# Optimization experiments

Measured on AMD Instinct MI355X. Metric: run time of the kernel, lower is better.

## Reference

```python
import jax, jax.numpy as jnp
import numpy as np

B, L, F = 8, 4096, 64  # batch, max_len, feat_dim (in_features == out_features)


def setup_inputs() -> dict:
    key = jax.random.key(0)
    k1, k2, k3, k4 = jax.random.split(key, 4)
    text = jax.random.normal(k1, (B, L, F), dtype=jnp.float32)
    adj = jax.random.uniform(k2, (B, L, L), dtype=jnp.float32)
    weight = jax.random.normal(k3, (F, F), dtype=jnp.float32) * (1.0 / np.sqrt(F))
    bias = jax.random.normal(k4, (F,), dtype=jnp.float32) * 0.01
    return {"text": text, "adj": adj, "weight": weight, "bias": bias}


def reference(text, adj, weight, bias):
    # Original: out[b,i,:] = sum_j adj[b,i,j] * (text[b,j,:] @ W) + bias
    # i.e. adj @ (text @ W) + bias, without the wasteful [B,L,L,F] intermediate.
    hidden = jnp.einsum('blf,fo->blo', text, weight)      # [B,L,F]
    out = jnp.einsum('bij,bjo->bio', adj, hidden)          # [B,L,F]
    return out + bias
```

## Files before the change

### kernel.cpp

```cpp
#include <hip/hip_runtime.h>
#include <hip/hip_bf16.h>

#define LDIM 4096
#define FDIM 64
#define BM 64
#define BK 256
#define NIT (LDIM / BK)
#define SAP 264

typedef __attribute__((ext_vector_type(8))) __bf16 bf16x8;
typedef __attribute__((ext_vector_type(4))) float f32x4;

__device__ __forceinline__ unsigned short f2bf(float f) {
    unsigned int u = __float_as_uint(f);
    u += 0x7fffu + ((u >> 16) & 1u);
    return (unsigned short)(u >> 16);
}

__global__ __launch_bounds__(256) void hidden_kernel(
    const float* __restrict__ text, const float* __restrict__ weight,
    unsigned short* __restrict__ hT)
{
    const int b  = blockIdx.x & 7;
    const int lc = blockIdx.x >> 3;
    const int l0 = lc * 64;
    __shared__ float sw[64 * 64];
    __shared__ float st[64 * 65];
    const int t = threadIdx.x;
    #pragma unroll
    for (int i = 0; i < 16; ++i) sw[t + i * 256] = weight[t + i * 256];
    const float* tp = text + ((size_t)b * LDIM + l0) * FDIM;
    #pragma unroll
    for (int i = 0; i < 16; ++i) {
        int idx = t + i * 256;
        st[(idx >> 6) * 65 + (idx & 63)] = tp[idx];
    }
    __syncthreads();
    const int l  = t & 63;
    const int o0 = (t >> 6) * 16;
    float acc[16];
    #pragma unroll
    for (int i = 0; i < 16; ++i) acc[i] = 0.f;
    for (int f = 0; f < 64; ++f) {
        float tv = st[l * 65 + f];
        #pragma unroll
        for (int i = 0; i < 16; ++i) acc[i] += tv * sw[f * 64 + o0 + i];
    }
    unsigned short* hp = hT + ((size_t)b * FDIM + o0) * LDIM + l0 + l;
    #pragma unroll
    for (int i = 0; i < 16; ++i) hp[(size_t)i * LDIM] = f2bf(acc[i]);
}

__global__ __launch_bounds__(256, 2) void gemm_kernel(
    const float* __restrict__ adj, const unsigned short* __restrict__ hT,
    const float* __restrict__ bias, float* __restrict__ out)
{
    const int b  = blockIdx.x & 7;
    const int mb = blockIdx.x >> 3;
    const int m0 = mb * BM;
    const int tid  = threadIdx.x;
    const int w    = tid >> 6;
    const int lane = tid & 63;

    __shared__ __align__(16) unsigned short sA[BM * SAP];
    __shared__ __align__(16) unsigned short sB[64 * SAP];

    const float*          abase = adj + ((size_t)b * LDIM + m0) * LDIM;
    const unsigned short* hbase = hT + (size_t)b * FDIM * LDIM;

    float4 aReg[16]; uint4 bReg[8];

    #pragma unroll
    for (int i = 0; i < 16; ++i) {
        int idx = i * 256 + tid;
        aReg[i] = *(const float4*)(abase + (size_t)(idx >> 6) * LDIM + (idx & 63) * 4);
    }
    #pragma unroll
    for (int i = 0; i < 8; ++i) {
        int idx = i * 256 + tid;
        bReg[i] = *(const uint4*)(hbase + (size_t)(idx >> 5) * LDIM + (idx & 31) * 8);
    }

    f32x4 acc[4];
    #pragma unroll
    for (int nf = 0; nf < 4; ++nf) acc[nf] = (f32x4){0.f, 0.f, 0.f, 0.f};

    const int fm = lane & 15;
    const int fq = lane >> 4;

    for (int it = 0; it < NIT; ++it) {
        __syncthreads();
        #pragma unroll
        for (int i = 0; i < 16; ++i) {
            int idx = i * 256 + tid;
            union { unsigned short us[4]; uint2 v; } pk;
            pk.us[0] = f2bf(aReg[i].x); pk.us[1] = f2bf(aReg[i].y);
            pk.us[2] = f2bf(aReg[i].z); pk.us[3] = f2bf(aReg[i].w);
            *(uint2*)&sA[(idx >> 6) * SAP + (idx & 63) * 4] = pk.v;
        }
        #pragma unroll
        for (int i = 0; i < 8; ++i) {
            int idx = i * 256 + tid;
            *(uint4*)&sB[(idx >> 5) * SAP + (idx & 31) * 8] = bReg[i];
        }
        __syncthreads();

        if (it + 1 < NIT) {
            const int k0 = (it + 1) * BK;
            #pragma unroll
            for (int i = 0; i < 16; ++i) {
                int idx = i * 256 + tid;
                aReg[i] = *(const float4*)(abase + (size_t)(idx >> 6) * LDIM + k0 + (idx & 63) * 4);
            }
            #pragma unroll
            for (int i = 0; i < 8; ++i) {
                int idx = i * 256 + tid;
                bReg[i] = *(const uint4*)(hbase + (size_t)(idx >> 5) * LDIM + k0 + (idx & 31) * 8);
            }
        }

        #pragma unroll
        for (int kf = 0; kf < 8; ++kf) {
            bf16x8 af = *(const bf16x8*)&sA[(w * 16 + fm) * SAP + kf * 32 + fq * 8];
            #pragma unroll
            for (int nf = 0; nf < 4; ++nf) {
                bf16x8 bfr = *(const bf16x8*)&sB[(nf * 16 + fm) * SAP + kf * 32 + fq * 8];
                acc[nf] = __builtin_amdgcn_mfma_f32_16x16x32_bf16(af, bfr, acc[nf], 0, 0, 0);
            }
        }
    }

    float* obase = out + ((size_t)b * LDIM + m0 + w * 16 + fq * 4) * FDIM + fm;
    #pragma unroll
    for (int nf = 0; nf < 4; ++nf) {
        float bv = bias[nf * 16 + fm];
        #pragma unroll
        for (int r = 0; r < 4; ++r)
            obase[(size_t)r * FDIM + nf * 16] = acc[nf][r] + bv;
    }
}

extern "C" void kernel_launch(void* const* d_in, const int* in_sizes, int n_in,
                              void* d_out, int out_size, void* d_ws, size_t ws_size,
                              hipStream_t stream) {
    const float* text   = (const float*)d_in[0];
    const float* adj    = (const float*)d_in[1];
    const float* weight = (const float*)d_in[2];
    const float* bias   = (const float*)d_in[3];
    float* out = (float*)d_out;
    unsigned short* hT = (unsigned short*)d_ws;

    hidden_kernel<<<512, 256, 0, stream>>>(text, weight, hT);
    gemm_kernel<<<512, 256, 0, stream>>>(adj, hT, bias, out);
}
```

Before: 737.8 us.

## Fuse text@W projection into adjacency GEMM with per-block recomputation

Removes the separate hidden-projection kernel and its bf16 workspace round trip, recomputing text@W per K-tile inside each GEMM block using MFMA with weights held in registers. Shared memory is reused between the text tile and the adj tile. This trades one launch and the workspace write/read for redundant projection work across all row blocks, doubled text reads, extra barriers and higher register pressure.

```diff
diff --git a/kernel.cpp b/kernel.cpp
--- a/kernel.cpp
+++ b/kernel.cpp
@@ -7,6 +7,7 @@
 #define BK 256
 #define NIT (LDIM / BK)
 #define SAP 264
+#define STP 72
 
 typedef __attribute__((ext_vector_type(8))) __bf16 bf16x8;
 typedef __attribute__((ext_vector_type(4))) float f32x4;
@@ -17,43 +18,10 @@
     return (unsigned short)(u >> 16);
 }
 
-__global__ __launch_bounds__(256) void hidden_kernel(
-    const float* __restrict__ text, const float* __restrict__ weight,
-    unsigned short* __restrict__ hT)
-{
-    const int b  = blockIdx.x & 7;
-    const int lc = blockIdx.x >> 3;
-    const int l0 = lc * 64;
-    __shared__ float sw[64 * 64];
-    __shared__ float st[64 * 65];
-    const int t = threadIdx.x;
-    #pragma unroll
-    for (int i = 0; i < 16; ++i) sw[t + i * 256] = weight[t + i * 256];
-    const float* tp = text + ((size_t)b * LDIM + l0) * FDIM;
-    #pragma unroll
-    for (int i = 0; i < 16; ++i) {
-        int idx = t + i * 256;
-        st[(idx >> 6) * 65 + (idx & 63)] = tp[idx];
-    }
-    __syncthreads();
-    const int l  = t & 63;
-    const int o0 = (t >> 6) * 16;
-    float acc[16];
-    #pragma unroll
-    for (int i = 0; i < 16; ++i) acc[i] = 0.f;
-    for (int f = 0; f < 64; ++f) {
-        float tv = st[l * 65 + f];
-        #pragma unroll
-        for (int i = 0; i < 16; ++i) acc[i] += tv * sw[f * 64 + o0 + i];
-    }
-    unsigned short* hp = hT + ((size_t)b * FDIM + o0) * LDIM + l0 + l;
-    #pragma unroll
-    for (int i = 0; i < 16; ++i) hp[(size_t)i * LDIM] = f2bf(acc[i]);
-}
-
-__global__ __launch_bounds__(256, 2) void gemm_kernel(
-    const float* __restrict__ adj, const unsigned short* __restrict__ hT,
-    const float* __restrict__ bias, float* __restrict__ out)
+__global__ __launch_bounds__(256, 2) void fused_kernel(
+    const float* __restrict__ text, const float* __restrict__ adj,
+    const float* __restrict__ weight, const float* __restrict__ bias,
+    float* __restrict__ out)
 {
     const int b  = blockIdx.x & 7;
     const int mb = blockIdx.x >> 3;
@@ -61,70 +29,114 @@
     const int tid  = threadIdx.x;
     const int w    = tid >> 6;
     const int lane = tid & 63;
+    const int fm = lane & 15;
+    const int fq = lane >> 4;
 
-    __shared__ __align__(16) unsigned short sA[BM * SAP];
-    __shared__ __align__(16) unsigned short sB[64 * SAP];
+    __shared__ __align__(16) unsigned short sTA[256 * STP];
+    __shared__ __align__(16) unsigned short sH[64 * SAP];
 
-    const float*          abase = adj + ((size_t)b * LDIM + m0) * LDIM;
-    const unsigned short* hbase = hT + (size_t)b * FDIM * LDIM;
+    const float* tbase = text + (size_t)b * LDIM * FDIM;
+    const float* abase = adj  + ((size_t)b * LDIM + m0) * LDIM;
 
-    float4 aReg[16]; uint4 bReg[8];
+    bf16x8 wB[2][4];
+    #pragma unroll
+    for (int fs = 0; fs < 2; ++fs)
+        #pragma unroll
+        for (int ob = 0; ob < 4; ++ob) {
+            union { unsigned short us[8]; bf16x8 v; } u8;
+            #pragma unroll
+            for (int j = 0; j < 8; ++j)
+                u8.us[j] = f2bf(weight[(size_t)(fs * 32 + fq * 8 + j) * FDIM + ob * 16 + fm]);
+            wB[fs][ob] = u8.v;
+        }
 
+    float4 tReg[16]; float4 aReg[16];
+    #pragma unroll
+    for (int i = 0; i < 16; ++i) {
+        int idx = i * 256 + tid;
+        tReg[i] = *(const float4*)(tbase + (size_t)(idx >> 4) * FDIM + (idx & 15) * 4);
+    }
     #pragma unroll
     for (int i = 0; i < 16; ++i) {
         int idx = i * 256 + tid;
         aReg[i] = *(const float4*)(abase + (size_t)(idx >> 6) * LDIM + (idx & 63) * 4);
-    }
-    #pragma unroll
-    for (int i = 0; i < 8; ++i) {
-        int idx = i * 256 + tid;
-        bReg[i] = *(const uint4*)(hbase + (size_t)(idx >> 5) * LDIM + (idx & 31) * 8);
     }
 
     f32x4 acc[4];
     #pragma unroll
     for (int nf = 0; nf < 4; ++nf) acc[nf] = (f32x4){0.f, 0.f, 0.f, 0.f};
 
-    const int fm = lane & 15;
-    const int fq = lane >> 4;
+    for (int it = 0; it < NIT; ++it) {
+        const bool more = (it + 1 < NIT);
+        const int  k0n  = (it + 1) * BK;
 
-    for (int it = 0; it < NIT; ++it) {
         __syncthreads();
+        #pragma unroll
+        for (int i = 0; i < 16; ++i) {
+            int idx = i * 256 + tid;
+            union { unsigned short us[4]; uint2 v; } pk;
+            pk.us[0] = f2bf(tReg[i].x); pk.us[1] = f2bf(tReg[i].y);
+            pk.us[2] = f2bf(tReg[i].z); pk.us[3] = f2bf(tReg[i].w);
+            *(uint2*)&sTA[(idx >> 4) * STP + (idx & 15) * 4] = pk.v;
+        }
+        __syncthreads();
+
+        if (more) {
+            #pragma unroll
+            for (int i = 0; i < 16; ++i) {
+                int idx = i * 256 + tid;
+                tReg[i] = *(const float4*)(tbase + (size_t)(k0n + (idx >> 4)) * FDIM + (idx & 15) * 4);
+            }
+        }
+
+        f32x4 acc2[4][4];
+        #pragma unroll
+        for (int i = 0; i < 4; ++i)
+            #pragma unroll
+            for (int ob = 0; ob < 4; ++ob) acc2[i][ob] = (f32x4){0.f, 0.f, 0.f, 0.f};
+        #pragma unroll
+        for (int fs = 0; fs < 2; ++fs)
+            #pragma unroll
+            for (int i = 0; i < 4; ++i) {
+                bf16x8 af = *(const bf16x8*)&sTA[(w * 64 + i * 16 + fm) * STP + fs * 32 + fq * 8];
+                #pragma unroll
+                for (int ob = 0; ob < 4; ++ob)
+                    acc2[i][ob] = __builtin_amdgcn_mfma_f32_16x16x32_bf16(af, wB[fs][ob], acc2[i][ob], 0, 0, 0);
+            }
+        __syncthreads();
+
         #pragma unroll
         for (int i = 0; i < 16; ++i) {
             int idx = i * 256 + tid;
             union { unsigned short us[4]; uint2 v; } pk;
             pk.us[0] = f2bf(aReg[i].x); pk.us[1] = f2bf(aReg[i].y);
             pk.us[2] = f2bf(aReg[i].z); pk.us[3] = f2bf(aReg[i].w);
-            *(uint2*)&sA[(idx >> 6) * SAP + (idx & 63) * 4] = pk.v;
+            *(uint2*)&sTA[(idx >> 6) * SAP + (idx & 63) * 4] = pk.v;
         }
         #pragma unroll
-        for (int i = 0; i < 8; ++i) {
-            int idx = i * 256 + tid;
-            *(uint4*)&sB[(idx >> 5) * SAP + (idx & 31) * 8] = bReg[i];
+        for (int i = 0; i < 4; ++i)
+            #pragma unroll
+            for (int ob = 0; ob < 4; ++ob) {
+                union { unsigned short us[4]; uint2 v; } pk;
+                pk.us[0] = f2bf(acc2[i][ob][0]); pk.us[1] = f2bf(acc2[i][ob][1]);
+                pk.us[2] = f2bf(acc2[i][ob][2]); pk.us[3] = f2bf(acc2[i][ob][3]);
+                *(uint2*)&sH[(ob * 16 + fm) * SAP + w * 64 + i * 16 + fq * 4] = pk.v;
+            }
+        if (more) {
+            #pragma unroll
+            for (int i = 0; i < 16; ++i) {
+                int idx = i * 256 + tid;
+                aReg[i] = *(const float4*)(abase + (size_t)(idx >> 6) * LDIM + k0n + (idx & 63) * 4);
+            }
         }
         __syncthreads();
 
-        if (it + 1 < NIT) {
-            const int k0 = (it + 1) * BK;
-            #pragma unroll
-            for (int i = 0; i < 16; ++i) {
-                int idx = i * 256 + tid;
-                aReg[i] = *(const float4*)(abase + (size_t)(idx >> 6) * LDIM + k0 + (idx & 63) * 4);
-            }
-            #pragma unroll
-            for (int i = 0; i < 8; ++i) {
-                int idx = i * 256 + tid;
-                bReg[i] = *(const uint4*)(hbase + (size_t)(idx >> 5) * LDIM + k0 + (idx & 31) * 8);
-            }
-        }
-
         #pragma unroll
         for (int kf = 0; kf < 8; ++kf) {
-            bf16x8 af = *(const bf16x8*)&sA[(w * 16 + fm) * SAP + kf * 32 + fq * 8];
+            bf16x8 af = *(const bf16x8*)&sTA[(w * 16 + fm) * SAP + kf * 32 + fq * 8];
             #pragma unroll
             for (int nf = 0; nf < 4; ++nf) {
-                bf16x8 bfr = *(const bf16x8*)&sB[(nf * 16 + fm) * SAP + kf * 32 + fq * 8];
+                bf16x8 bfr = *(const bf16x8*)&sH[(nf * 16 + fm) * SAP + kf * 32 + fq * 8];
                 acc[nf] = __builtin_amdgcn_mfma_f32_16x16x32_bf16(af, bfr, acc[nf], 0, 0, 0);
             }
         }
@@ -148,8 +160,7 @@
     const float* weight = (const float*)d_in[2];
     const float* bias   = (const float*)d_in[3];
     float* out = (float*)d_out;
-    unsigned short* hT = (unsigned short*)d_ws;
+    (void)d_ws; (void)ws_size;
 
-    hidden_kernel<<<512, 256, 0, stream>>>(text, weight, hT);
-    gemm_kernel<<<512, 256, 0, stream>>>(adj, hT, bias, out);
+    fused_kernel<<<512, 256, 0, stream>>>(text, adj, weight, bias, out);
 }
```

New measurement: 946.7 us. 28.3% more time.

## Split-K the adjacency GEMM into quarters with a separate bias-reduce kernel

Applied to the files above, without the earlier changes.

The adjacency GEMM now splits the K dimension into four 1024-wide chunks and uses 16-row tiles, raising the grid from 512 to 8192 blocks. Each block loads its whole A tile into LDS once and streams hidden-feature fragments straight from global memory into registers with double buffering, so there is no per-iteration LDS staging of B. The four partial results go to workspace and a new reduce kernel sums them and adds the bias. This aims to improve occupancy and memory-level parallelism on the bandwidth-bound adj read, at the cost of extra partial-sum traffic and an additional kernel launch.

```diff
diff --git a/kernel.cpp b/kernel.cpp
--- a/kernel.cpp
+++ b/kernel.cpp
@@ -3,10 +3,10 @@
 
 #define LDIM 4096
 #define FDIM 64
-#define BM 64
-#define BK 256
-#define NIT (LDIM / BK)
-#define SAP 264
+#define KQLEN 1024
+#define BROWS 16
+#define SAP2 1032
+#define PQ_F4 524288
 
 typedef __attribute__((ext_vector_type(8))) __bf16 bf16x8;
 typedef __attribute__((ext_vector_type(4))) float f32x4;
@@ -51,93 +51,88 @@
     for (int i = 0; i < 16; ++i) hp[(size_t)i * LDIM] = f2bf(acc[i]);
 }
 
-__global__ __launch_bounds__(256, 2) void gemm_kernel(
+__global__ __launch_bounds__(256) void gemm_kernel(
     const float* __restrict__ adj, const unsigned short* __restrict__ hT,
-    const float* __restrict__ bias, float* __restrict__ out)
+    float* __restrict__ part)
 {
     const int b  = blockIdx.x & 7;
-    const int mb = blockIdx.x >> 3;
-    const int m0 = mb * BM;
+    const int kq = (blockIdx.x >> 3) & 3;
+    const int mb = blockIdx.x >> 5;
+    const int m0 = mb * BROWS;
+    const int k0 = kq * KQLEN;
     const int tid  = threadIdx.x;
     const int w    = tid >> 6;
     const int lane = tid & 63;
+    const int fm = lane & 15;
+    const int fq = lane >> 4;
 
-    __shared__ __align__(16) unsigned short sA[BM * SAP];
-    __shared__ __align__(16) unsigned short sB[64 * SAP];
+    __shared__ __align__(16) unsigned short sA[BROWS * SAP2];
 
-    const float*          abase = adj + ((size_t)b * LDIM + m0) * LDIM;
-    const unsigned short* hbase = hT + (size_t)b * FDIM * LDIM;
+    const float* abase = adj + ((size_t)b * LDIM + m0) * LDIM + k0;
 
-    float4 aReg[16]; uint4 bReg[8];
-
+    float4 aReg[16];
     #pragma unroll
     for (int i = 0; i < 16; ++i) {
         int idx = i * 256 + tid;
-        aReg[i] = *(const float4*)(abase + (size_t)(idx >> 6) * LDIM + (idx & 63) * 4);
+        aReg[i] = *(const float4*)(abase + (size_t)(idx >> 8) * LDIM + (idx & 255) * 4);
     }
     #pragma unroll
-    for (int i = 0; i < 8; ++i) {
+    for (int i = 0; i < 16; ++i) {
         int idx = i * 256 + tid;
-        bReg[i] = *(const uint4*)(hbase + (size_t)(idx >> 5) * LDIM + (idx & 31) * 8);
+        union { unsigned short us[4]; uint2 v; } pk;
+        pk.us[0] = f2bf(aReg[i].x); pk.us[1] = f2bf(aReg[i].y);
+        pk.us[2] = f2bf(aReg[i].z); pk.us[3] = f2bf(aReg[i].w);
+        *(uint2*)&sA[(idx >> 8) * SAP2 + (idx & 255) * 4] = pk.v;
     }
+    __syncthreads();
 
-    f32x4 acc[4];
+    const unsigned short* hrow = hT + (size_t)b * FDIM * LDIM
+                               + (size_t)(w * 16 + fm) * LDIM + k0 + fq * 8;
+    bf16x8 bReg[2][8];
     #pragma unroll
-    for (int nf = 0; nf < 4; ++nf) acc[nf] = (f32x4){0.f, 0.f, 0.f, 0.f};
+    for (int j = 0; j < 8; ++j)
+        bReg[0][j] = *(const bf16x8*)(hrow + j * 32);
 
-    const int fm = lane & 15;
-    const int fq = lane >> 4;
-
-    for (int it = 0; it < NIT; ++it) {
-        __syncthreads();
-        #pragma unroll
-        for (int i = 0; i < 16; ++i) {
-            int idx = i * 256 + tid;
-            union { unsigned short us[4]; uint2 v; } pk;
-            pk.us[0] = f2bf(aReg[i].x); pk.us[1] = f2bf(aReg[i].y);
-            pk.us[2] = f2bf(aReg[i].z); pk.us[3] = f2bf(aReg[i].w);
-            *(uint2*)&sA[(idx >> 6) * SAP + (idx & 63) * 4] = pk.v;
+    f32x4 acc = (f32x4){0.f, 0.f, 0.f, 0.f};
+    #pragma unroll
+    for (int g = 0; g < 4; ++g) {
+        const int cur = g & 1, nxt = cur ^ 1;
+        if (g < 3) {
+            #pragma unroll
+            for (int j = 0; j < 8; ++j)
+                bReg[nxt][j] = *(const bf16x8*)(hrow + ((g + 1) * 8 + j) * 32);
         }
         #pragma unroll
-        for (int i = 0; i < 8; ++i) {
-            int idx = i * 256 + tid;
-            *(uint4*)&sB[(idx >> 5) * SAP + (idx & 31) * 8] = bReg[i];
-        }
-        __syncthreads();
-
-        if (it + 1 < NIT) {
-            const int k0 = (it + 1) * BK;
-            #pragma unroll
-            for (int i = 0; i < 16; ++i) {
-                int idx = i * 256 + tid;
-                aReg[i] = *(const float4*)(abase + (size_t)(idx >> 6) * LDIM + k0 + (idx & 63) * 4);
-            }
-            #pragma unroll
-            for (int i = 0; i < 8; ++i) {
-                int idx = i * 256 + tid;
-                bReg[i] = *(const uint4*)(hbase + (size_t)(idx >> 5) * LDIM + k0 + (idx & 31) * 8);
-            }
-        }
-
-        #pragma unroll
-        for (int kf = 0; kf < 8; ++kf) {
-            bf16x8 af = *(const bf16x8*)&sA[(w * 16 + fm) * SAP + kf * 32 + fq * 8];
-            #pragma unroll
-            for (int nf = 0; nf < 4; ++nf) {
-                bf16x8 bfr = *(const bf16x8*)&sB[(nf * 16 + fm) * SAP + kf * 32 + fq * 8];
-                acc[nf] = __builtin_amdgcn_mfma_f32_16x16x32_bf16(af, bfr, acc[nf], 0, 0, 0);
-            }
+        for (int j = 0; j < 8; ++j) {
+            const int kf = g * 8 + j;
+            bf16x8 af = *(const bf16x8*)&sA[fm * SAP2 + kf * 32 + fq * 8];
+            acc = __builtin_amdgcn_mfma_f32_16x16x32_bf16(af, bReg[cur][j], acc, 0, 0, 0);
         }
     }
 
-    float* obase = out + ((size_t)b * LDIM + m0 + w * 16 + fq * 4) * FDIM + fm;
+    float* pbase = part + (((size_t)kq * 8 + b) * LDIM + m0 + fq * 4) * FDIM + w * 16 + fm;
     #pragma unroll
-    for (int nf = 0; nf < 4; ++nf) {
-        float bv = bias[nf * 16 + fm];
-        #pragma unroll
-        for (int r = 0; r < 4; ++r)
-            obase[(size_t)r * FDIM + nf * 16] = acc[nf][r] + bv;
-    }
+    for (int r = 0; r < 4; ++r)
+        pbase[(size_t)r * FDIM] = acc[r];
+}
+
+__global__ __launch_bounds__(256) void reduce_kernel(
+    const float* __restrict__ part, const float* __restrict__ bias,
+    float* __restrict__ out)
+{
+    const size_t i = (size_t)blockIdx.x * 256 + threadIdx.x;
+    const float4* p = (const float4*)part;
+    float4 a = p[i];
+    float4 c = p[i + PQ_F4];
+    float4 d = p[i + 2 * (size_t)PQ_F4];
+    float4 e = p[i + 3 * (size_t)PQ_F4];
+    float4 bv = *(const float4*)(bias + ((i & 15) << 2));
+    float4 r;
+    r.x = a.x + c.x + d.x + e.x + bv.x;
+    r.y = a.y + c.y + d.y + e.y + bv.y;
+    r.z = a.z + c.z + d.z + e.z + bv.z;
+    r.w = a.w + c.w + d.w + e.w + bv.w;
+    ((float4*)out)[i] = r;
 }
 
 extern "C" void kernel_launch(void* const* d_in, const int* in_sizes, int n_in,
@@ -149,7 +144,9 @@
     const float* bias   = (const float*)d_in[3];
     float* out = (float*)d_out;
     unsigned short* hT = (unsigned short*)d_ws;
+    float* part = (float*)((char*)d_ws + (8u << 20));
 
     hidden_kernel<<<512, 256, 0, stream>>>(text, weight, hT);
-    gemm_kernel<<<512, 256, 0, stream>>>(adj, hT, bias, out);
+    gemm_kernel<<<8192, 256, 0, stream>>>(adj, hT, part);
+    reduce_kernel<<<2048, 256, 0, stream>>>(part, bias, out);
 }
```

New measurement: 742.0 us. Within noise of the previous version (+0.6%).
